# Optimization experiments

Hardware: AMD Instinct MI355X
Metric: run time of the kernel (lower is better)

The kernel has to match this reference:

```python
import jax, jax.numpy as jnp
import numpy as np

N_NODES = 100000
H_FEATS = 128
N_TRIPLETS = 500000


def setup_inputs() -> dict:
    key = jax.random.key(0)
    k_h, k_t, k_w1, k_b1, k_w2, k_b2 = jax.random.split(key, 6)
    h = jax.random.normal(k_h, (N_NODES, H_FEATS), dtype=jnp.float32)
    triplets = jax.random.randint(k_t, (N_TRIPLETS, 3), 0, N_NODES, dtype=jnp.int64)
    # nn.Linear weights: [out, in]
    W1_w = jax.random.normal(k_w1, (H_FEATS, 3 * H_FEATS), dtype=jnp.float32) * 0.05
    W1_b = jax.random.normal(k_b1, (H_FEATS,), dtype=jnp.float32) * 0.05
    W2_w = jax.random.normal(k_w2, (2, H_FEATS), dtype=jnp.float32) * 0.05
    W2_b = jax.random.normal(k_b2, (2,), dtype=jnp.float32) * 0.05
    return {"h": h, "triplets": triplets, "W1_w": W1_w, "W1_b": W1_b,
            "W2_w": W2_w, "W2_b": W2_b}


def reference(h, triplets, W1_w, W1_b, W2_w, W2_b):
    # gather: [T, 3, H] -> [T, 3*H]
    T = triplets.shape[0]
    emb = h[triplets].reshape(T, 3 * H_FEATS)
    hid = jax.nn.relu(emb @ W1_w.T + W1_b)   # [T, H]
    out = hid @ W2_w.T + W2_b                # [T, 2]
    return out
```

## Files before the change

kernel.cpp:

```cpp
#include <hip/hip_runtime.h>

typedef __bf16 bf16x8 __attribute__((ext_vector_type(8)));
typedef float f32x4 __attribute__((ext_vector_type(4)));

__device__ __forceinline__ unsigned short f2bf(float x) {
  union { float f; unsigned int i; } u; u.f = x;
  return (unsigned short)((u.i + 0x7FFFu + ((u.i >> 16) & 1u)) >> 16);
}
__device__ __forceinline__ float bf2f(unsigned short b) {
  union { unsigned int i; float f; } u; u.i = ((unsigned int)b) << 16;
  return u.f;
}
__device__ __forceinline__ bf16x8 cvt8(float4 a, float4 b) {
  union { unsigned short u[8]; bf16x8 v; } r;
  r.u[0] = f2bf(a.x); r.u[1] = f2bf(a.y); r.u[2] = f2bf(a.z); r.u[3] = f2bf(a.w);
  r.u[4] = f2bf(b.x); r.u[5] = f2bf(b.y); r.u[6] = f2bf(b.z); r.u[7] = f2bf(b.w);
  return r.v;
}

__global__ void pack_w1_kernel(const float* __restrict__ W1w, uint4* __restrict__ wp) {
  int fid = blockIdx.x * 256 + threadIdx.x;
  int kk = fid / 1536;
  int rem = fid - kk * 1536;
  int nf = rem >> 6;
  int ln = rem & 63;
  int ng = nf * 16 + (ln & 15);
  int c = ng & 127;
  int jp = ng >> 7;
  int k0 = kk * 32 + (ln >> 4) * 8;
  const float* src = W1w + (size_t)c * 384 + jp * 128 + k0;
  float4 a = *(const float4*)src;
  float4 b = *(const float4*)(src + 4);
  union { unsigned short u[8]; uint4 v; } r;
  r.u[0] = f2bf(a.x); r.u[1] = f2bf(a.y); r.u[2] = f2bf(a.z); r.u[3] = f2bf(a.w);
  r.u[4] = f2bf(b.x); r.u[5] = f2bf(b.y); r.u[6] = f2bf(b.z); r.u[7] = f2bf(b.w);
  wp[fid] = r.v;
}

__global__ __launch_bounds__(1024) void phaseA_kernel(
    const float* __restrict__ h, const uint4* __restrict__ wp,
    unsigned short* __restrict__ P, int Nn) {
  extern __shared__ uint4 wl[];
  const int tid = threadIdx.x;
  for (int i = tid; i < 6144; i += 1024) wl[i] = wp[i];
  __syncthreads();

  const int lane = tid & 63;
  const int wv = tid >> 6;
  const int rg = wv >> 2;
  const int cg = wv & 3;
  const int l15 = lane & 15;
  const int lg = lane >> 4;
  const int mb = blockIdx.x * 64 + rg * 16;

  int arow = mb + l15;
  if (arow >= Nn) arow = Nn - 1;
  const float* ap = h + (size_t)arow * 128 + lg * 8;

  f32x4 acc[6];
#pragma unroll
  for (int nf = 0; nf < 6; nf++) acc[nf] = (f32x4){0.f, 0.f, 0.f, 0.f};

#pragma unroll
  for (int kk = 0; kk < 4; kk++) {
    bf16x8 af = cvt8(*(const float4*)(ap + kk * 32), *(const float4*)(ap + kk * 32 + 4));
#pragma unroll
    for (int nf = 0; nf < 6; nf++) {
      bf16x8 bf = __builtin_bit_cast(bf16x8, wl[(kk * 24 + cg * 6 + nf) * 64 + lane]);
      acc[nf] = __builtin_amdgcn_mfma_f32_16x16x32_bf16(af, bf, acc[nf], 0, 0, 0);
    }
  }
#pragma unroll
  for (int nf = 0; nf < 6; nf++) {
#pragma unroll
    for (int r = 0; r < 4; r++) {
      int row = mb + lg * 4 + r;
      if (row < Nn) P[(size_t)row * 384 + (cg * 6 + nf) * 16 + l15] = f2bf(acc[nf][r]);
    }
  }
}

__global__ __launch_bounds__(256) void phaseB_kernel(
    const unsigned short* __restrict__ P, const int* __restrict__ trip,
    const float* __restrict__ b1, const float* __restrict__ W2w,
    const float* __restrict__ b2, float* __restrict__ out, int T) {
  const int gtid = blockIdx.x * 256 + threadIdx.x;
  const int g0 = gtid >> 4;
  const int c8 = threadIdx.x & 15;
  const int ng = (gridDim.x * 256) >> 4;
  const int c0 = c8 * 8;

  float4 b1a = *(const float4*)(b1 + c0), b1b = *(const float4*)(b1 + c0 + 4);
  float4 w0a = *(const float4*)(W2w + c0), w0b = *(const float4*)(W2w + c0 + 4);
  float4 w1a = *(const float4*)(W2w + 128 + c0), w1b = *(const float4*)(W2w + 128 + c0 + 4);
  const float bb0 = b2[0], bb1 = b2[1];
  float b1r[8] = {b1a.x, b1a.y, b1a.z, b1a.w, b1b.x, b1b.y, b1b.z, b1b.w};
  float w20[8] = {w0a.x, w0a.y, w0a.z, w0a.w, w0b.x, w0b.y, w0b.z, w0b.w};
  float w21[8] = {w1a.x, w1a.y, w1a.z, w1a.w, w1b.x, w1b.y, w1b.z, w1b.w};

  for (int t = g0; t < T; t += 4 * ng) {
    int tc[4];
    bool hv[4];
#pragma unroll
    for (int u = 0; u < 4; u++) {
      int tt = t + u * ng;
      hv[u] = tt < T;
      tc[u] = hv[u] ? tt : t;
    }
    union { uint4 v; unsigned short u[8]; } va[4][3];
#pragma unroll
    for (int u = 0; u < 4; u++) {
      int i0 = trip[3 * tc[u]], i1 = trip[3 * tc[u] + 1], i2 = trip[3 * tc[u] + 2];
      va[u][0].v = *((const uint4*)(P + (size_t)i0 * 384) + c8);
      va[u][1].v = *((const uint4*)(P + (size_t)i1 * 384 + 128) + c8);
      va[u][2].v = *((const uint4*)(P + (size_t)i2 * 384 + 256) + c8);
    }
    float p0[4], p1[4];
#pragma unroll
    for (int u = 0; u < 4; u++) {
      p0[u] = 0.f; p1[u] = 0.f;
#pragma unroll
      for (int j = 0; j < 8; j++) {
        float s = bf2f(va[u][0].u[j]) + bf2f(va[u][1].u[j]) + bf2f(va[u][2].u[j]) + b1r[j];
        s = fmaxf(s, 0.f);
        p0[u] = fmaf(s, w20[j], p0[u]);
        p1[u] = fmaf(s, w21[j], p1[u]);
      }
    }
#pragma unroll
    for (int d = 1; d < 16; d <<= 1) {
#pragma unroll
      for (int u = 0; u < 4; u++) {
        p0[u] += __shfl_xor(p0[u], d);
        p1[u] += __shfl_xor(p1[u], d);
      }
    }
    if (c8 == 0) {
#pragma unroll
      for (int u = 0; u < 4; u++) {
        if (hv[u]) {
          float2 o;
          o.x = p0[u] + bb0;
          o.y = p1[u] + bb1;
          *(float2*)(out + (size_t)(t + u * ng) * 2) = o;
        }
      }
    }
  }
}

__global__ __launch_bounds__(512, 2) void fused_fallback(
    const float* __restrict__ Hsrc, const int* __restrict__ trip,
    const float* __restrict__ W1w, const float* __restrict__ b1,
    const float* __restrict__ W2w, const float* __restrict__ b2,
    float* __restrict__ out, int T) {
  extern __shared__ unsigned short w1p[];
  const int tid = threadIdx.x;
  for (int f = tid; f < 6144; f += 512) {
    int kk = f >> 9; int nf = (f >> 6) & 7; int ln = f & 63;
    int row = nf * 16 + (ln & 15); int k0 = kk * 32 + (ln >> 4) * 8;
    const float* src = W1w + row * 384 + k0;
    float4 a = *(const float4*)src; float4 b = *(const float4*)(src + 4);
    union { unsigned short u[8]; uint4 v; } r;
    r.u[0] = f2bf(a.x); r.u[1] = f2bf(a.y); r.u[2] = f2bf(a.z); r.u[3] = f2bf(a.w);
    r.u[4] = f2bf(b.x); r.u[5] = f2bf(b.y); r.u[6] = f2bf(b.z); r.u[7] = f2bf(b.w);
    *(uint4*)&w1p[f * 8] = r.v;
  }
  __syncthreads();
  const int lane = tid & 63, wv = tid >> 6, l15 = lane & 15, lg = lane >> 4;
  float b1r[8], w20[8], w21[8];
#pragma unroll
  for (int nf = 0; nf < 8; nf++) {
    int c = nf * 16 + l15;
    b1r[nf] = b1[c]; w20[nf] = W2w[c]; w21[nf] = W2w[128 + c];
  }
  const float bb0 = b2[0], bb1 = b2[1];
  const int ntiles = (T + 511) >> 9;
  for (int tile = blockIdx.x; tile < ntiles; tile += gridDim.x) {
    const int base = tile * 512 + wv * 64;
    f32x4 acc[4][8];
#pragma unroll
    for (int m = 0; m < 4; m++)
#pragma unroll
      for (int nf = 0; nf < 8; nf++) acc[m][nf] = (f32x4){0.f, 0.f, 0.f, 0.f};
    int off[4][3];
#pragma unroll
    for (int m = 0; m < 4; m++) {
      int row = base + m * 16 + l15;
      int rc = row < T ? row : T - 1;
      off[m][0] = trip[rc * 3]; off[m][1] = trip[rc * 3 + 1]; off[m][2] = trip[rc * 3 + 2];
    }
#pragma unroll
    for (int part = 0; part < 3; part++)
#pragma unroll
      for (int kq = 0; kq < 4; kq++) {
        const int kk = part * 4 + kq;
        bf16x8 af[4];
#pragma unroll
        for (int m = 0; m < 4; m++) {
          const float* p = Hsrc + ((size_t)off[m][part] << 7) + kq * 32 + lg * 8;
          af[m] = cvt8(*(const float4*)p, *(const float4*)(p + 4));
        }
#pragma unroll
        for (int nf = 0; nf < 8; nf++) {
          bf16x8 bf = __builtin_bit_cast(bf16x8,
              *(const uint4*)&w1p[(size_t)(kk * 512 + nf * 64 + lane) * 8]);
#pragma unroll
          for (int m = 0; m < 4; m++)
            acc[m][nf] = __builtin_amdgcn_mfma_f32_16x16x32_bf16(af[m], bf, acc[m][nf], 0, 0, 0);
        }
      }
#pragma unroll
    for (int m = 0; m < 4; m++) {
      float p0[4] = {0, 0, 0, 0}, p1[4] = {0, 0, 0, 0};
#pragma unroll
      for (int nf = 0; nf < 8; nf++)
#pragma unroll
        for (int r = 0; r < 4; r++) {
          float hv = fmaxf(acc[m][nf][r] + b1r[nf], 0.f);
          p0[r] = fmaf(hv, w20[nf], p0[r]);
          p1[r] = fmaf(hv, w21[nf], p1[r]);
        }
#pragma unroll
      for (int d = 1; d < 16; d <<= 1)
#pragma unroll
        for (int r = 0; r < 4; r++) {
          p0[r] += __shfl_xor(p0[r], d);
          p1[r] += __shfl_xor(p1[r], d);
        }
#pragma unroll
      for (int r = 0; r < 4; r++)
        if (l15 == r) {
          int row = base + m * 16 + lg * 4 + r;
          if (row < T) {
            float2 o; o.x = p0[r] + bb0; o.y = p1[r] + bb1;
            *(float2*)(out + (size_t)row * 2) = o;
          }
        }
    }
  }
}

extern "C" void kernel_launch(void* const* d_in, const int* in_sizes, int n_in,
                              void* d_out, int out_size, void* d_ws, size_t ws_size,
                              hipStream_t stream) {
  const float* h = (const float*)d_in[0];
  const int* trip = (const int*)d_in[1];
  const float* W1w = (const float*)d_in[2];
  const float* b1 = (const float*)d_in[3];
  const float* W2w = (const float*)d_in[4];
  const float* b2 = (const float*)d_in[5];
  float* out = (float*)d_out;

  const int Nn = in_sizes[0] / 128;
  const int T = in_sizes[1] / 3;
  const size_t pbytes = (size_t)Nn * 384 * 2;
  const size_t need = pbytes + 6144 * 16;

  if (ws_size >= need) {
    unsigned short* P = (unsigned short*)d_ws;
    uint4* wp = (uint4*)((char*)d_ws + pbytes);
    pack_w1_kernel<<<24, 256, 0, stream>>>(W1w, wp);
    phaseA_kernel<<<(Nn + 63) / 64, 1024, 6144 * 16, stream>>>(h, wp, P, Nn);
    phaseB_kernel<<<2048, 256, 0, stream>>>(P, trip, b1, W2w, b2, out, T);
  } else {
    fused_fallback<<<256, 512, 6144 * 16, stream>>>(h, trip, W1w, b1, W2w, b2, out, T);
  }
}
```

Baseline: 111.5 us.

## Keep W1 fragments in registers with persistent phaseA, drop pack kernel

The separate W1 packing kernel and its LDS staging are removed. Each wave of a persistent 512-block phaseA grid now converts its 48-column slice of W1 to bf16 once and keeps it in registers, then loops over 32-row tiles of h. This saves one kernel launch, the LDS fill and the barrier per block, at the cost of higher register pressure and each block redundantly reading W1 from global memory. PhaseB's gather unroll also goes from 4 to 5 triplets per iteration to keep more loads in flight.

```diff
diff --git a/kernel.cpp b/kernel.cpp
--- a/kernel.cpp
+++ b/kernel.cpp
@@ -18,65 +18,66 @@
   return r.v;
 }
 
-__global__ void pack_w1_kernel(const float* __restrict__ W1w, uint4* __restrict__ wp) {
-  int fid = blockIdx.x * 256 + threadIdx.x;
-  int kk = fid / 1536;
-  int rem = fid - kk * 1536;
-  int nf = rem >> 6;
-  int ln = rem & 63;
-  int ng = nf * 16 + (ln & 15);
-  int c = ng & 127;
-  int jp = ng >> 7;
-  int k0 = kk * 32 + (ln >> 4) * 8;
-  const float* src = W1w + (size_t)c * 384 + jp * 128 + k0;
-  float4 a = *(const float4*)src;
-  float4 b = *(const float4*)(src + 4);
-  union { unsigned short u[8]; uint4 v; } r;
-  r.u[0] = f2bf(a.x); r.u[1] = f2bf(a.y); r.u[2] = f2bf(a.z); r.u[3] = f2bf(a.w);
-  r.u[4] = f2bf(b.x); r.u[5] = f2bf(b.y); r.u[6] = f2bf(b.z); r.u[7] = f2bf(b.w);
-  wp[fid] = r.v;
-}
-
-__global__ __launch_bounds__(1024) void phaseA_kernel(
-    const float* __restrict__ h, const uint4* __restrict__ wp,
+__global__ __launch_bounds__(512, 4) void phaseA_kernel(
+    const float* __restrict__ h, const float* __restrict__ W1w,
     unsigned short* __restrict__ P, int Nn) {
-  extern __shared__ uint4 wl[];
   const int tid = threadIdx.x;
-  for (int i = tid; i < 6144; i += 1024) wl[i] = wp[i];
-  __syncthreads();
-
   const int lane = tid & 63;
-  const int wv = tid >> 6;
-  const int rg = wv >> 2;
-  const int cg = wv & 3;
+  const int cg = tid >> 6;
   const int l15 = lane & 15;
   const int lg = lane >> 4;
-  const int mb = blockIdx.x * 64 + rg * 16;
-
-  int arow = mb + l15;
-  if (arow >= Nn) arow = Nn - 1;
-  const float* ap = h + (size_t)arow * 128 + lg * 8;
-
-  f32x4 acc[6];
-#pragma unroll
-  for (int nf = 0; nf < 6; nf++) acc[nf] = (f32x4){0.f, 0.f, 0.f, 0.f};
-
-#pragma unroll
-  for (int kk = 0; kk < 4; kk++) {
-    bf16x8 af = cvt8(*(const float4*)(ap + kk * 32), *(const float4*)(ap + kk * 32 + 4));
-#pragma unroll
-    for (int nf = 0; nf < 6; nf++) {
-      bf16x8 bf = __builtin_bit_cast(bf16x8, wl[(kk * 24 + cg * 6 + nf) * 64 + lane]);
-      acc[nf] = __builtin_amdgcn_mfma_f32_16x16x32_bf16(af, bf, acc[nf], 0, 0, 0);
-    }
-  }
-#pragma unroll
-  for (int nf = 0; nf < 6; nf++) {
-#pragma unroll
-    for (int r = 0; r < 4; r++) {
-      int row = mb + lg * 4 + r;
-      if (row < Nn) P[(size_t)row * 384 + (cg * 6 + nf) * 16 + l15] = f2bf(acc[nf][r]);
-    }
+
+  bf16x8 bfr[3][4];
+#pragma unroll
+  for (int nf = 0; nf < 3; nf++) {
+    const int ng = cg * 48 + nf * 16 + l15;
+    const int c = ng & 127, jp = ng >> 7;
+    const float* wsrc = W1w + (size_t)c * 384 + jp * 128 + lg * 8;
+#pragma unroll
+    for (int kk = 0; kk < 4; kk++)
+      bfr[nf][kk] = cvt8(*(const float4*)(wsrc + kk * 32),
+                         *(const float4*)(wsrc + kk * 32 + 4));
+  }
+
+  const int ntiles = (Nn + 31) >> 5;
+  for (int tile = blockIdx.x; tile < ntiles; tile += gridDim.x) {
+    const int r0 = tile * 32;
+    const float* ap[2];
+#pragma unroll
+    for (int m = 0; m < 2; m++) {
+      int arow = r0 + m * 16 + l15;
+      if (arow >= Nn) arow = Nn - 1;
+      ap[m] = h + (size_t)arow * 128 + lg * 8;
+    }
+    f32x4 acc[2][3];
+#pragma unroll
+    for (int m = 0; m < 2; m++)
+#pragma unroll
+      for (int nf = 0; nf < 3; nf++) acc[m][nf] = (f32x4){0.f, 0.f, 0.f, 0.f};
+
+#pragma unroll
+    for (int kk = 0; kk < 4; kk++) {
+      bf16x8 af[2];
+#pragma unroll
+      for (int m = 0; m < 2; m++)
+        af[m] = cvt8(*(const float4*)(ap[m] + kk * 32),
+                     *(const float4*)(ap[m] + kk * 32 + 4));
+#pragma unroll
+      for (int m = 0; m < 2; m++)
+#pragma unroll
+        for (int nf = 0; nf < 3; nf++)
+          acc[m][nf] = __builtin_amdgcn_mfma_f32_16x16x32_bf16(af[m], bfr[nf][kk], acc[m][nf], 0, 0, 0);
+    }
+#pragma unroll
+    for (int m = 0; m < 2; m++)
+#pragma unroll
+      for (int nf = 0; nf < 3; nf++)
+#pragma unroll
+        for (int r = 0; r < 4; r++) {
+          int row = r0 + m * 16 + lg * 4 + r;
+          if (row < Nn)
+            P[(size_t)row * 384 + cg * 48 + nf * 16 + l15] = f2bf(acc[m][nf][r]);
+        }
   }
 }
 
@@ -84,6 +85,7 @@
     const unsigned short* __restrict__ P, const int* __restrict__ trip,
     const float* __restrict__ b1, const float* __restrict__ W2w,
     const float* __restrict__ b2, float* __restrict__ out, int T) {
+  constexpr int U = 5;
   const int gtid = blockIdx.x * 256 + threadIdx.x;
   const int g0 = gtid >> 4;
   const int c8 = threadIdx.x & 15;
@@ -98,26 +100,26 @@
   float w20[8] = {w0a.x, w0a.y, w0a.z, w0a.w, w0b.x, w0b.y, w0b.z, w0b.w};
   float w21[8] = {w1a.x, w1a.y, w1a.z, w1a.w, w1b.x, w1b.y, w1b.z, w1b.w};
 
-  for (int t = g0; t < T; t += 4 * ng) {
-    int tc[4];
-    bool hv[4];
-#pragma unroll
-    for (int u = 0; u < 4; u++) {
+  for (int t = g0; t < T; t += U * ng) {
+    int tc[U];
+    bool hv[U];
+#pragma unroll
+    for (int u = 0; u < U; u++) {
       int tt = t + u * ng;
       hv[u] = tt < T;
       tc[u] = hv[u] ? tt : t;
     }
-    union { uint4 v; unsigned short u[8]; } va[4][3];
-#pragma unroll
-    for (int u = 0; u < 4; u++) {
+    union { uint4 v; unsigned short u[8]; } va[U][3];
+#pragma unroll
+    for (int u = 0; u < U; u++) {
       int i0 = trip[3 * tc[u]], i1 = trip[3 * tc[u] + 1], i2 = trip[3 * tc[u] + 2];
       va[u][0].v = *((const uint4*)(P + (size_t)i0 * 384) + c8);
       va[u][1].v = *((const uint4*)(P + (size_t)i1 * 384 + 128) + c8);
       va[u][2].v = *((const uint4*)(P + (size_t)i2 * 384 + 256) + c8);
     }
-    float p0[4], p1[4];
-#pragma unroll
-    for (int u = 0; u < 4; u++) {
+    float p0[U], p1[U];
+#pragma unroll
+    for (int u = 0; u < U; u++) {
       p0[u] = 0.f; p1[u] = 0.f;
 #pragma unroll
       for (int j = 0; j < 8; j++) {
@@ -130,14 +132,14 @@
 #pragma unroll
     for (int d = 1; d < 16; d <<= 1) {
 #pragma unroll
-      for (int u = 0; u < 4; u++) {
+      for (int u = 0; u < U; u++) {
         p0[u] += __shfl_xor(p0[u], d);
         p1[u] += __shfl_xor(p1[u], d);
       }
     }
     if (c8 == 0) {
 #pragma unroll
-      for (int u = 0; u < 4; u++) {
+      for (int u = 0; u < U; u++) {
         if (hv[u]) {
           float2 o;
           o.x = p0[u] + bb0;
@@ -255,13 +257,10 @@
   const int Nn = in_sizes[0] / 128;
   const int T = in_sizes[1] / 3;
   const size_t pbytes = (size_t)Nn * 384 * 2;
-  const size_t need = pbytes + 6144 * 16;
-
-  if (ws_size >= need) {
+
+  if (ws_size >= pbytes) {
     unsigned short* P = (unsigned short*)d_ws;
-    uint4* wp = (uint4*)((char*)d_ws + pbytes);
-    pack_w1_kernel<<<24, 256, 0, stream>>>(W1w, wp);
-    phaseA_kernel<<<(Nn + 63) / 64, 1024, 6144 * 16, stream>>>(h, wp, P, Nn);
+    phaseA_kernel<<<512, 512, 0, stream>>>(h, W1w, P, Nn);
     phaseB_kernel<<<2048, 256, 0, stream>>>(P, trip, b1, W2w, b2, out, T);
   } else {
     fused_fallback<<<256, 512, 6144 * 16, stream>>>(h, trip, W1w, b1, W2w, b2, out, T);
```

Measured after the change: 124.8 us. 1.12x slower.
